# Performance work log

Measured on AMD Instinct MI355X. Metric: run time of the kernel, lower is better.

Reference implementation:

```python
import jax, jax.numpy as jnp
import numpy as np

N = 20000   # genes
E = 200000  # global edges
P = 300     # pathways
EP = 2000   # edges per pathway (global node indices)
D = 3       # in_dim == number of omics (forced by nn.Linear(3,1))


def setup_inputs():
    key = jax.random.key(0)
    ks = jax.random.split(key, 20)
    f = lambda i, shape: jax.random.normal(ks[i], shape, dtype=jnp.float32) * 0.1
    return {
        "x": f(0, (N, D)),
        "edge_index": jax.random.randint(ks[1], (2, E), 0, N),
        "path_edges": jax.random.randint(ks[2], (P, 2, EP), 0, N),
        "W_pool": f(3, (D, D)), "b_pool": f(4, (D,)),
        "W_self": f(5, (D, D)), "W_neigh": f(6, (D, D)), "b_conv": f(7, (D,)),
        "sub_Wl": f(8, (P, D, D)), "sub_bl": f(9, (P, D)), "sub_Wr": f(10, (P, D, D)),
        "pool_Wrel": f(11, (P, D, 1)), "pool_Wroot": f(12, (P, D, 1)), "pool_b": f(13, (P, 1)),
        "gate_W": f(14, (P, D, 1)), "gate_b": f(15, (P, 1)),
        "lin_W": f(16, (D, 1)), "lin_b": f(17, (1,)),
        "mlp_W": f(18, (P, 1)), "mlp_b": f(19, (1,)),
    }


def reference(x, edge_index, path_edges, W_pool, b_pool, W_self, W_neigh, b_conv,
              sub_Wl, sub_bl, sub_Wr, pool_Wrel, pool_Wroot, pool_b,
              gate_W, gate_b, lin_W, lin_b, mlp_W, mlp_b):
    n = x.shape[0]
    # add_self_loops on the global edge_index
    loops = jnp.arange(n)
    src = jnp.concatenate([edge_index[0], loops])
    dst = jnp.concatenate([edge_index[1], loops])

    # global SAGEConv with 'pool' aggregator: max_j relu(W_pool h_j), then self + neigh
    hp = jax.nn.relu(x @ W_pool + b_pool)                       # [N,D]
    agg = jax.ops.segment_max(hp[src], dst, num_segments=n)     # [N,D] (self-loops -> no empty segments)
    h = jnp.tanh(x @ W_self + agg @ W_neigh + b_conv)           # [N,D]

    k = int(np.ceil(0.8 * n))  # SAGPooling ratio=0.8 over all N nodes (full x is passed per pathway)

    def per_path(pe, Wl, bl, Wr, Wrel, Wroot, pb, gW, gb):
        s, d = pe[0], pe[1]
        # SAGEConv (mean aggr) on pathway subgraph edges over full node set
        msum = jax.ops.segment_sum(h[s], d, num_segments=n)
        cnt = jax.ops.segment_sum(jnp.ones(s.shape, h.dtype), d, num_segments=n)
        mean = msum / jnp.maximum(cnt, 1.0)[:, None]
        xc = jax.nn.relu(mean @ Wl + bl + h @ Wr)               # [N,D]
        # SAGPooling score via GraphConv (add aggr): W_rel * sum_j x_j + W_root * x + b
        asum = jax.ops.segment_sum(xc[s], d, num_segments=n)
        score = (asum @ Wrel + xc @ Wroot + pb)[:, 0]           # [N]
        topv, perm = jax.lax.top_k(score, k)
        xk = xc[perm] * jnp.tanh(topv)[:, None]                 # [k,D]
        # GlobalAttention readout: softmax gate over kept nodes
        gate = jax.nn.softmax((xk @ gW + gb)[:, 0])             # [k]
        return jax.nn.relu(gate @ xk)                            # [D]

    readout = jax.vmap(per_path)(path_edges, sub_Wl, sub_bl, sub_Wr,
                                 pool_Wrel, pool_Wroot, pool_b, gate_W, gate_b)  # [P,D]
    r = jax.nn.relu(readout @ lin_W + lin_b).T                  # [1,P]
    # mlp: Dropout (identity in eval) -> ReLU -> Linear(P,1) -> Sigmoid
    return jax.nn.sigmoid(jax.nn.relu(r) @ mlp_W + mlp_b)       # [1,1]
```

## Files before the change

### kernel.cpp

```cpp
#include <hip/hip_runtime.h>
#include <math.h>

#define MAXM 2048
#define BMW  640
#define BS   1024
#define NPT  20
#define NB   2048

__device__ __forceinline__ unsigned fkey(float f){
  unsigned u = __float_as_uint(f);
  return (u & 0x80000000u) ? ~u : (u | 0x80000000u);
}
__device__ __forceinline__ int lbin(float sc, float lo, float scl){
  int b = (int)((sc - lo) * scl);
  return b < 0 ? 0 : (b > NB-1 ? NB-1 : b);
}
__device__ __forceinline__ void hp_eval(const float* __restrict__ x, int i,
                                        const float* __restrict__ Wp,
                                        const float* __restrict__ bp, float* o){
  float x0 = x[i*3+0], x1 = x[i*3+1], x2 = x[i*3+2];
  #pragma unroll
  for (int j = 0; j < 3; ++j)
    o[j] = fmaxf(x0*Wp[0*3+j] + x1*Wp[1*3+j] + x2*Wp[2*3+j] + bp[j], 0.f);
}

__global__ void k_edge(const float* __restrict__ x, const int* __restrict__ ei,
                       const float* __restrict__ Wp, const float* __restrict__ bp,
                       float* __restrict__ agg, float* __restrict__ acc,
                       unsigned* __restrict__ counter, int E){
  if (blockIdx.x == 0 && threadIdx.x == 0){ acc[0] = 0.f; counter[0] = 0u; }
  int e = blockIdx.x*blockDim.x + threadIdx.x;
  if (e >= E) return;
  int s = ei[e], d = ei[E+e];
  float o[3]; hp_eval(x, s, Wp, bp, o);
  #pragma unroll
  for (int j = 0; j < 3; ++j)
    atomicMax((int*)&agg[d*3+j], __float_as_int(o[j]));
}

__global__ void k_h2(const float* __restrict__ x, const float* __restrict__ agg,
                     float4* __restrict__ h4,
                     const float* __restrict__ Wp, const float* __restrict__ bp,
                     const float* __restrict__ Ws, const float* __restrict__ Wn,
                     const float* __restrict__ bc, int N){
  int i = blockIdx.x*blockDim.x + threadIdx.x;
  if (i >= N) return;
  float hp[3]; hp_eval(x, i, Wp, bp, hp);
  float x0 = x[i*3+0], x1 = x[i*3+1], x2 = x[i*3+2];
  float a0 = fmaxf(agg[i*3+0], hp[0]);
  float a1 = fmaxf(agg[i*3+1], hp[1]);
  float a2 = fmaxf(agg[i*3+2], hp[2]);
  float o[3];
  #pragma unroll
  for (int j = 0; j < 3; ++j){
    float v = x0*Ws[0*3+j] + x1*Ws[1*3+j] + x2*Ws[2*3+j]
            + a0*Wn[0*3+j] + a1*Wn[1*3+j] + a2*Wn[2*3+j] + bc[j];
    o[j] = tanhf(v);
  }
  h4[i] = make_float4(o[0], o[1], o[2], 0.f);
}

__device__ __forceinline__ void pick_bucket(const unsigned* hist, int l,
    unsigned pref, unsigned mask, int shift,
    unsigned* sel_prefix, unsigned* sel_mask, int* sel_r){
  unsigned h0 = hist[4*l+0], h1 = hist[4*l+1], h2 = hist[4*l+2], h3 = hist[4*l+3];
  unsigned s = h0+h1+h2+h3;
  unsigned S = s;
  #pragma unroll
  for (int off = 1; off < 64; off <<= 1){
    unsigned t = __shfl_down(S, off);
    if (l + off < 64) S += t;
  }
  unsigned Snext = S - s;
  unsigned r = (unsigned)*sel_r;
  unsigned suf3 = h3 + Snext;
  unsigned suf2 = h2 + suf3;
  unsigned suf1 = h1 + suf2;
  unsigned suf0 = h0 + suf1;
  int b = -1; unsigned sufnext = 0;
  if      (suf3 >= r && Snext < r){ b = 4*l+3; sufnext = Snext; }
  else if (suf2 >= r && suf3  < r){ b = 4*l+2; sufnext = suf3; }
  else if (suf1 >= r && suf2  < r){ b = 4*l+1; sufnext = suf2; }
  else if (suf0 >= r && suf1  < r){ b = 4*l+0; sufnext = suf1; }
  if (b >= 0){
    *sel_prefix = pref | ((unsigned)b << shift);
    *sel_mask   = mask | (255u << shift);
    *sel_r      = (int)(r - sufnext);
  }
}

__global__ void __launch_bounds__(BS, 4)
k_mega(const float4* __restrict__ h4, const int* __restrict__ pe,
       const float* __restrict__ sWl, const float* __restrict__ sbl, const float* __restrict__ sWr,
       const float* __restrict__ pWrel, const float* __restrict__ pWroot, const float* __restrict__ pB,
       const float* __restrict__ gW, const float* __restrict__ gB,
       const float* __restrict__ linW, const float* __restrict__ linb,
       const float* __restrict__ mlpW, const float* __restrict__ mlpb,
       float* __restrict__ spG, float* __restrict__ acc, unsigned* __restrict__ counter,
       unsigned* __restrict__ out, int N, int EP, int K, int P){
  __shared__ unsigned bm[BMW];
  __shared__ int      wpfx[BMW];
  __shared__ float    msum[MAXM*3];
  __shared__ unsigned scrA[NB];
  __shared__ unsigned scrB[NB];
  __shared__ float    wredf[(BS/64)*4];
  __shared__ float    s_mn, s_mx;
  __shared__ float    rlo[3], rsc[3];
  __shared__ int      rb[3];
  __shared__ int      s_r, s_C, s_cc, s_done;
  __shared__ unsigned s_uT;
  __shared__ unsigned sel_prefix, sel_mask;
  __shared__ int      sel_r;

  const int p = blockIdx.x;
  const int tid = threadIdx.x;

  float Wl[9], Wr[9], bl[3], wrel[3], wroot[3], gw[3];
  #pragma unroll
  for (int j = 0; j < 9; ++j){ Wl[j] = sWl[p*9+j]; Wr[j] = sWr[p*9+j]; }
  #pragma unroll
  for (int j = 0; j < 3; ++j){
    bl[j] = sbl[p*3+j]; wrel[j] = pWrel[p*3+j];
    wroot[j] = pWroot[p*3+j]; gw[j] = gW[p*3+j];
  }
  float pbv = pB[p], gbv = gB[p];
  float* sp = spG + (size_t)p*N;

  int*   cnt  = (int*)scrA;
  float* adot = (float*)scrB;

  for (int s = tid; s < MAXM; s += BS){
    cnt[s] = 0; adot[s] = 0.f;
    msum[s*3+0]=0.f; msum[s*3+1]=0.f; msum[s*3+2]=0.f;
  }
  for (int s = tid; s < BMW; s += BS) bm[s] = 0u;
  if (tid == 0){ s_done = 0; s_uT = 0u; }
  __syncthreads();

  const int* ps = pe + (size_t)p*2*EP;
  const int* pd = ps + EP;

  for (int e = tid; e < EP; e += BS) atomicOr(&bm[pd[e]>>5], 1u << (pd[e]&31));
  __syncthreads();
  if (tid < 64){
    int l = tid, base = l*10;
    int c[10], s = 0;
    #pragma unroll
    for (int q = 0; q < 10; ++q){ c[q] = __popc(bm[base+q]); s += c[q]; }
    int pre = s;
    #pragma unroll
    for (int off = 1; off < 64; off <<= 1){
      int t = __shfl_up(pre, off);
      if (l >= off) pre += t;
    }
    pre -= s;
    #pragma unroll
    for (int q = 0; q < 10; ++q){ wpfx[base+q] = pre; pre += c[q]; }
  }
  __syncthreads();
  for (int e = tid; e < EP; e += BS){
    int s = ps[e], d = pd[e];
    int r = wpfx[d>>5] + __popc(bm[d>>5] & ((1u << (d&31)) - 1u));
    float4 hv = h4[s];
    atomicAdd(&cnt[r], 1);
    atomicAdd(&msum[r*3+0], hv.x);
    atomicAdd(&msum[r*3+1], hv.y);
    atomicAdd(&msum[r*3+2], hv.z);
  }
  __syncthreads();
  for (int r = tid; r < MAXM; r += BS){
    int c = cnt[r];
    if (c > 0){
      float inv = 1.f / (float)c;
      msum[r*3+0] *= inv; msum[r*3+1] *= inv; msum[r*3+2] *= inv;
    }
  }
  __syncthreads();
  for (int e = tid; e < EP; e += BS){
    int s = ps[e], d = pd[e];
    float m0=0.f,m1=0.f,m2=0.f;
    unsigned w = bm[s>>5];
    if ((w >> (s&31)) & 1u){
      int rs = wpfx[s>>5] + __popc(w & ((1u << (s&31)) - 1u));
      m0 = msum[rs*3+0]; m1 = msum[rs*3+1]; m2 = msum[rs*3+2];
    }
    float4 hv = h4[s];
    float x0 = fmaxf(m0*Wl[0]+m1*Wl[3]+m2*Wl[6] + bl[0] + hv.x*Wr[0]+hv.y*Wr[3]+hv.z*Wr[6], 0.f);
    float x1 = fmaxf(m0*Wl[1]+m1*Wl[4]+m2*Wl[7] + bl[1] + hv.x*Wr[1]+hv.y*Wr[4]+hv.z*Wr[7], 0.f);
    float x2 = fmaxf(m0*Wl[2]+m1*Wl[5]+m2*Wl[8] + bl[2] + hv.x*Wr[2]+hv.y*Wr[5]+hv.z*Wr[8], 0.f);
    int rd = wpfx[d>>5] + __popc(bm[d>>5] & ((1u << (d&31)) - 1u));
    atomicAdd(&adot[rd], x0*wrel[0] + x1*wrel[1] + x2*wrel[2]);
  }
  __syncthreads();

  float scq[NPT];
  float mn = 3.0e38f, mx = -3.0e38f;
  #pragma unroll
  for (int j = 0; j < NPT; ++j){
    int i = tid + j*BS;
    float sc = 0.f;
    if (i < N){
      float m0=0.f,m1=0.f,m2=0.f,ad=0.f;
      unsigned w = bm[i>>5];
      if ((w >> (i&31)) & 1u){
        int r = wpfx[i>>5] + __popc(w & ((1u << (i&31)) - 1u));
        m0 = msum[r*3+0]; m1 = msum[r*3+1]; m2 = msum[r*3+2];
        ad = adot[r];
      }
      float4 hv = h4[i];
      float x0 = fmaxf(m0*Wl[0]+m1*Wl[3]+m2*Wl[6] + bl[0] + hv.x*Wr[0]+hv.y*Wr[3]+hv.z*Wr[6], 0.f);
      float x1 = fmaxf(m0*Wl[1]+m1*Wl[4]+m2*Wl[7] + bl[1] + hv.x*Wr[1]+hv.y*Wr[4]+hv.z*Wr[7], 0.f);
      float x2 = fmaxf(m0*Wl[2]+m1*Wl[5]+m2*Wl[8] + bl[2] + hv.x*Wr[2]+hv.y*Wr[5]+hv.z*Wr[8], 0.f);
      sc = ad + x0*wroot[0]+x1*wroot[1]+x2*wroot[2] + pbv;
      mn = fminf(mn, sc); mx = fmaxf(mx, sc);
    }
    scq[j] = sc;
  }
  for (int i = BS*NPT + tid; i < N; i += BS){
    float m0=0.f,m1=0.f,m2=0.f,ad=0.f;
    unsigned w = bm[i>>5];
    if ((w >> (i&31)) & 1u){
      int r = wpfx[i>>5] + __popc(w & ((1u << (i&31)) - 1u));
      m0 = msum[r*3+0]; m1 = msum[r*3+1]; m2 = msum[r*3+2];
      ad = adot[r];
    }
    float4 hv = h4[i];
    float x0 = fmaxf(m0*Wl[0]+m1*Wl[3]+m2*Wl[6] + bl[0] + hv.x*Wr[0]+hv.y*Wr[3]+hv.z*Wr[6], 0.f);
    float x1 = fmaxf(m0*Wl[1]+m1*Wl[4]+m2*Wl[7] + bl[1] + hv.x*Wr[1]+hv.y*Wr[4]+hv.z*Wr[7], 0.f);
    float x2 = fmaxf(m0*Wl[2]+m1*Wl[5]+m2*Wl[8] + bl[2] + hv.x*Wr[2]+hv.y*Wr[5]+hv.z*Wr[8], 0.f);
    float sc = ad + x0*wroot[0]+x1*wroot[1]+x2*wroot[2] + pbv;
    sp[i] = sc;
    mn = fminf(mn, sc); mx = fmaxf(mx, sc);
  }
  #pragma unroll
  for (int off = 32; off > 0; off >>= 1){
    mn = fminf(mn, __shfl_down(mn, off));
    mx = fmaxf(mx, __shfl_down(mx, off));
  }
  if ((tid & 63) == 0){ int w = tid>>6; wredf[w*2+0] = mn; wredf[w*2+1] = mx; }
  __syncthreads();
  if (tid == 0){
    float a = 3.0e38f, b = -3.0e38f;
    for (int w = 0; w < BS/64; ++w){ a = fminf(a, wredf[w*2+0]); b = fmaxf(b, wredf[w*2+1]); }
    s_mn = a; s_mx = b; s_r = K;
    if (!(b > a)){ s_uT = fkey(a); s_done = 1; }
  }
  __syncthreads();

  unsigned* hist = scrA;
  unsigned* cand = scrB;

  for (int t = 0; t < 3; ++t){
    __syncthreads();
    if (s_done) break;
    float lo, hi;
    if (t == 0){ lo = s_mn; hi = s_mx; }
    else { lo = rlo[t-1] + rb[t-1]/rsc[t-1]; hi = rlo[t-1] + (rb[t-1]+1)/rsc[t-1]; }
    float scl = 2047.0f / (hi - lo);
    if (!(hi > lo) || !(scl < 1e37f)){
      if (tid == 0){ s_uT = fkey(lo); s_done = 1; }
      __syncthreads();
      continue;
    }
    for (int b = tid; b < NB; b += BS) hist[b] = 0u;
    __syncthreads();
    #pragma unroll
    for (int j = 0; j < NPT; ++j){
      int i = tid + j*BS;
      if (i < N){
        float sc = scq[j];
        bool act = true;
        for (int q = 0; q < t; ++q) act = act && (lbin(sc, rlo[q], rsc[q]) == rb[q]);
        if (act) atomicAdd(&hist[lbin(sc, lo, scl)], 1u);
      }
    }
    for (int i = BS*NPT + tid; i < N; i += BS){
      float sc = sp[i];
      bool act = true;
      for (int q = 0; q < t; ++q) act = act && (lbin(sc, rlo[q], rsc[q]) == rb[q]);
      if (act) atomicAdd(&hist[lbin(sc, lo, scl)], 1u);
    }
    __syncthreads();
    if (tid < 64){
      int l = tid;
      unsigned s = 0;
      for (int q = 0; q < 32; ++q) s += hist[l*32+q];
      unsigned S = s;
      #pragma unroll
      for (int off = 1; off < 64; off <<= 1){
        unsigned u2 = __shfl_down(S, off);
        if (l + off < 64) S += u2;
      }
      unsigned suf = S - s;
      unsigned r = (unsigned)s_r;
      int b = -1; unsigned sufnext = 0, cb = 0;
      for (int q = 31; q >= 0; --q){
        unsigned c = hist[l*32+q];
        unsigned nsuf = suf + c;
        if (nsuf >= r && suf < r){ b = l*32+q; sufnext = suf; cb = c; }
        suf = nsuf;
      }
      if (b >= 0){
        rb[t] = b; rlo[t] = lo; rsc[t] = scl;
        s_r = (int)(r - sufnext);
        s_C = (int)cb;
      }
    }
    __syncthreads();
    int C = s_C;
    if (C <= NB){
      if (tid == 0) s_cc = 0;
      __syncthreads();
      #pragma unroll
      for (int j = 0; j < NPT; ++j){
        int i = tid + j*BS;
        if (i < N){
          float sc = scq[j];
          bool act = true;
          for (int q = 0; q <= t; ++q) act = act && (lbin(sc, rlo[q], rsc[q]) == rb[q]);
          if (act){ int ix = atomicAdd(&s_cc, 1); if (ix < NB) cand[ix] = fkey(sc); }
        }
      }
      for (int i = BS*NPT + tid; i < N; i += BS){
        float sc = sp[i];
        bool act = true;
        for (int q = 0; q <= t; ++q) act = act && (lbin(sc, rlo[q], rsc[q]) == rb[q]);
        if (act){ int ix = atomicAdd(&s_cc, 1); if (ix < NB) cand[ix] = fkey(sc); }
      }
      __syncthreads();
      if (tid == 0){ sel_prefix = 0u; sel_mask = 0u; sel_r = s_r; }
      __syncthreads();
      for (int pass = 0; pass < 4; ++pass){
        int shift = 24 - 8*pass;
        if (tid < 256) hist[tid] = 0u;
        __syncthreads();
        unsigned mask = sel_mask, pref = sel_prefix;
        for (int j = tid; j < C; j += BS){
          unsigned u = cand[j];
          if ((u & mask) == pref) atomicAdd(&hist[(u>>shift)&255u], 1u);
        }
        __syncthreads();
        if (tid < 64)
          pick_bucket(hist, tid, pref, mask, shift, &sel_prefix, &sel_mask, &sel_r);
        __syncthreads();
      }
      if (tid == 0){ s_uT = sel_prefix; s_done = 1; }
      __syncthreads();
    } else if (t == 2){
      if (tid == 0){ s_uT = fkey(lo + rb[t]/scl); s_done = 1; }
      __syncthreads();
    }
  }
  __syncthreads();
  const unsigned uT = s_uT;

  float l = 0.f, a0 = 0.f, a1 = 0.f, a2 = 0.f;
  #pragma unroll
  for (int j = 0; j < NPT; ++j){
    int i = tid + j*BS;
    if (i < N && fkey(scq[j]) >= uT){
      float sc = scq[j];
      float m0=0.f,m1=0.f,m2=0.f;
      unsigned w = bm[i>>5];
      if ((w >> (i&31)) & 1u){
        int r = wpfx[i>>5] + __popc(w & ((1u << (i&31)) - 1u));
        m0 = msum[r*3+0]; m1 = msum[r*3+1]; m2 = msum[r*3+2];
      }
      float4 hv = h4[i];
      float x0 = fmaxf(m0*Wl[0]+m1*Wl[3]+m2*Wl[6] + bl[0] + hv.x*Wr[0]+hv.y*Wr[3]+hv.z*Wr[6], 0.f);
      float x1 = fmaxf(m0*Wl[1]+m1*Wl[4]+m2*Wl[7] + bl[1] + hv.x*Wr[1]+hv.y*Wr[4]+hv.z*Wr[7], 0.f);
      float x2 = fmaxf(m0*Wl[2]+m1*Wl[5]+m2*Wl[8] + bl[2] + hv.x*Wr[2]+hv.y*Wr[5]+hv.z*Wr[8], 0.f);
      float tt = tanhf(sc);
      x0 *= tt; x1 *= tt; x2 *= tt;
      float g = x0*gw[0] + x1*gw[1] + x2*gw[2] + gbv;
      g = fminf(fmaxf(g, -60.f), 60.f);
      float e = expf(g);
      l += e; a0 += e*x0; a1 += e*x1; a2 += e*x2;
    }
  }
  for (int i = BS*NPT + tid; i < N; i += BS){
    float sc = sp[i];
    if (fkey(sc) >= uT){
      float m0=0.f,m1=0.f,m2=0.f;
      unsigned w = bm[i>>5];
      if ((w >> (i&31)) & 1u){
        int r = wpfx[i>>5] + __popc(w & ((1u << (i&31)) - 1u));
        m0 = msum[r*3+0]; m1 = msum[r*3+1]; m2 = msum[r*3+2];
      }
      float4 hv = h4[i];
      float x0 = fmaxf(m0*Wl[0]+m1*Wl[3]+m2*Wl[6] + bl[0] + hv.x*Wr[0]+hv.y*Wr[3]+hv.z*Wr[6], 0.f);
      float x1 = fmaxf(m0*Wl[1]+m1*Wl[4]+m2*Wl[7] + bl[1] + hv.x*Wr[1]+hv.y*Wr[4]+hv.z*Wr[7], 0.f);
      float x2 = fmaxf(m0*Wl[2]+m1*Wl[5]+m2*Wl[8] + bl[2] + hv.x*Wr[2]+hv.y*Wr[5]+hv.z*Wr[8], 0.f);
      float tt = tanhf(sc);
      x0 *= tt; x1 *= tt; x2 *= tt;
      float g = x0*gw[0] + x1*gw[1] + x2*gw[2] + gbv;
      g = fminf(fmaxf(g, -60.f), 60.f);
      float e = expf(g);
      l += e; a0 += e*x0; a1 += e*x1; a2 += e*x2;
    }
  }
  #pragma unroll
  for (int off = 32; off > 0; off >>= 1){
    l  += __shfl_down(l,  off);
    a0 += __shfl_down(a0, off);
    a1 += __shfl_down(a1, off);
    a2 += __shfl_down(a2, off);
  }
  if ((tid & 63) == 0){
    int w = tid >> 6;
    wredf[w*4+0]=l; wredf[w*4+1]=a0; wredf[w*4+2]=a1; wredf[w*4+3]=a2;
  }
  __syncthreads();
  if (tid == 0){
    float L=0.f, A0=0.f, A1=0.f, A2=0.f;
    for (int w = 0; w < BS/64; ++w){
      L += wredf[w*4+0]; A0 += wredf[w*4+1]; A1 += wredf[w*4+2]; A2 += wredf[w*4+3];
    }
    float inv = 1.f / L;
    float r0 = fmaxf(A0*inv, 0.f);
    float r1 = fmaxf(A1*inv, 0.f);
    float r2 = fmaxf(A2*inv, 0.f);
    float rr = fmaxf(r0*linW[0] + r1*linW[1] + r2*linW[2] + linb[0], 0.f);
    atomicAdd(acc, rr * mlpW[p]);
    __threadfence();
    unsigned old = atomicAdd(counter, 1u);
    if (old == (unsigned)(P-1)){
      __threadfence();
      float z = atomicAdd(acc, 0.f) + mlpb[0];
      float a = 1.f / (1.f + expf(-z));
      unsigned A = __float_as_uint(a);
      unsigned B = (A + 0x7FFFu + ((A >> 16) & 1u)) >> 16;
      out[0] = (A & 0xFFFF0000u) | (B & 0xFFFFu);
    }
  }
}

extern "C" void kernel_launch(void* const* d_in, const int* in_sizes, int n_in,
                              void* d_out, int out_size, void* d_ws, size_t ws_size,
                              hipStream_t stream){
  const float* x      = (const float*)d_in[0];
  const int*   ei     = (const int*)  d_in[1];
  const int*   pe     = (const int*)  d_in[2];
  const float* W_pool = (const float*)d_in[3];
  const float* b_pool = (const float*)d_in[4];
  const float* W_self = (const float*)d_in[5];
  const float* W_neigh= (const float*)d_in[6];
  const float* b_conv = (const float*)d_in[7];
  const float* sWl    = (const float*)d_in[8];
  const float* sbl    = (const float*)d_in[9];
  const float* sWr    = (const float*)d_in[10];
  const float* pWrel  = (const float*)d_in[11];
  const float* pWroot = (const float*)d_in[12];
  const float* pB     = (const float*)d_in[13];
  const float* gW     = (const float*)d_in[14];
  const float* gB     = (const float*)d_in[15];
  const float* linW   = (const float*)d_in[16];
  const float* linb   = (const float*)d_in[17];
  const float* mlpW   = (const float*)d_in[18];
  const float* mlpb   = (const float*)d_in[19];

  const int N  = in_sizes[0] / 3;
  const int E  = in_sizes[1] / 2;
  const int P  = in_sizes[13];
  const int EP = in_sizes[2] / (2 * P);
  const int K  = (4*N + 4) / 5;

  float*    ws      = (float*)d_ws;
  float*    acc     = ws;
  unsigned* counter = (unsigned*)(ws + 1);
  float*    agg     = ws + 16;
  size_t    o_h4    = (16 + (size_t)3*N + 3) & ~(size_t)3;
  float4*   h4      = (float4*)(ws + o_h4);
  float*    spG     = ws + o_h4 + (size_t)4*N;

  k_edge<<<(E+255)/256, 256, 0, stream>>>(x, ei, W_pool, b_pool, agg, acc, counter, E);
  k_h2  <<<(N+255)/256, 256, 0, stream>>>(x, agg, h4, W_pool, b_pool,
                                          W_self, W_neigh, b_conv, N);
  k_mega<<<P, BS, 0, stream>>>(h4, pe, sWl, sbl, sWr, pWrel, pWroot, pB, gW, gB,
                               linW, linb, mlpW, mlpb,
                               spG, acc, counter, (unsigned*)d_out, N, EP, K, P);
}
```

Before: 256.1 us.

## Shrink per-block LDS in pathway kernel to fit more blocks per CU

Cuts the pathway kernel's shared memory by moving per-node edge counts to a global buffer (zeroed by a memset), storing mean features as bf16 in a reused region, shortening the prefix table to 16-bit, and halving the histogram bins. Block size drops to 512 threads with 40 scores per thread in registers. The goal is lower LDS per block so more of the 300 pathway blocks stay resident per CU. The cost is global atomics for counts, bf16 rounding error on the mean features, coarser top-k binning that may need more refinement passes, and higher register pressure from the larger per-thread score array.

```diff
diff --git a/kernel.cpp b/kernel.cpp
--- a/kernel.cpp
+++ b/kernel.cpp
@@ -1,11 +1,11 @@
 #include <hip/hip_runtime.h>
 #include <math.h>
 
-#define MAXM 2048
+#define MAXM 2000
 #define BMW  640
-#define BS   1024
-#define NPT  20
-#define NB   2048
+#define BS   512
+#define NPT  40
+#define NB   1024
 
 __device__ __forceinline__ unsigned fkey(float f){
   unsigned u = __float_as_uint(f);
@@ -14,6 +14,13 @@
 __device__ __forceinline__ int lbin(float sc, float lo, float scl){
   int b = (int)((sc - lo) * scl);
   return b < 0 ? 0 : (b > NB-1 ? NB-1 : b);
+}
+__device__ __forceinline__ unsigned short benc(float f){
+  unsigned A = __float_as_uint(f);
+  return (unsigned short)((A + 0x7FFFu + ((A >> 16) & 1u)) >> 16);
+}
+__device__ __forceinline__ float bdec(unsigned short u){
+  return __uint_as_float(((unsigned)u) << 16);
 }
 __device__ __forceinline__ void hp_eval(const float* __restrict__ x, int i,
                                         const float* __restrict__ Wp,
@@ -96,21 +103,17 @@
        const float* __restrict__ gW, const float* __restrict__ gB,
        const float* __restrict__ linW, const float* __restrict__ linb,
        const float* __restrict__ mlpW, const float* __restrict__ mlpb,
-       float* __restrict__ spG, float* __restrict__ acc, unsigned* __restrict__ counter,
+       int* __restrict__ cntG, float* __restrict__ spG,
+       float* __restrict__ acc, unsigned* __restrict__ counter,
        unsigned* __restrict__ out, int N, int EP, int K, int P){
-  __shared__ unsigned bm[BMW];
-  __shared__ int      wpfx[BMW];
-  __shared__ float    msum[MAXM*3];
-  __shared__ unsigned scrA[NB];
-  __shared__ unsigned scrB[NB];
-  __shared__ float    wredf[(BS/64)*4];
-  __shared__ float    s_mn, s_mx;
-  __shared__ float    rlo[3], rsc[3];
-  __shared__ int      rb[3];
-  __shared__ int      s_r, s_C, s_cc, s_done;
-  __shared__ unsigned s_uT;
-  __shared__ unsigned sel_prefix, sel_mask;
-  __shared__ int      sel_r;
+  __shared__ unsigned       bm[BMW];
+  __shared__ unsigned short wpfx[BMW];
+  __shared__ float          Xf[6000];
+  __shared__ float          wredf[64];
+  __shared__ float s_mn, s_mx, rlo[3], rsc[3];
+  __shared__ int   rb[3], s_r, s_C, s_cc, s_done;
+  __shared__ unsigned s_uT, sel_prefix, sel_mask;
+  __shared__ int   sel_r;
 
   const int p = blockIdx.x;
   const int tid = threadIdx.x;
@@ -125,14 +128,15 @@
   }
   float pbv = pB[p], gbv = gB[p];
   float* sp = spG + (size_t)p*N;
-
-  int*   cnt  = (int*)scrA;
-  float* adot = (float*)scrB;
-
-  for (int s = tid; s < MAXM; s += BS){
-    cnt[s] = 0; adot[s] = 0.f;
-    msum[s*3+0]=0.f; msum[s*3+1]=0.f; msum[s*3+2]=0.f;
-  }
+  int*   cntP = cntG + (size_t)p*MAXM;
+
+  float*          msum  = Xf;
+  unsigned short* msumh = (unsigned short*)Xf;
+  float*          adot  = Xf + 3000;
+  unsigned*       hist  = (unsigned*)(Xf + 3000);
+  unsigned*       cand  = (unsigned*)(Xf + 3000) + NB;
+
+  for (int s = tid; s < 6000; s += BS) msum[s] = 0.f;
   for (int s = tid; s < BMW; s += BS) bm[s] = 0u;
   if (tid == 0){ s_done = 0; s_uT = 0u; }
   __syncthreads();
@@ -155,25 +159,37 @@
     }
     pre -= s;
     #pragma unroll
-    for (int q = 0; q < 10; ++q){ wpfx[base+q] = pre; pre += c[q]; }
+    for (int q = 0; q < 10; ++q){ wpfx[base+q] = (unsigned short)pre; pre += c[q]; }
   }
   __syncthreads();
   for (int e = tid; e < EP; e += BS){
     int s = ps[e], d = pd[e];
-    int r = wpfx[d>>5] + __popc(bm[d>>5] & ((1u << (d&31)) - 1u));
+    int r = (int)wpfx[d>>5] + __popc(bm[d>>5] & ((1u << (d&31)) - 1u));
     float4 hv = h4[s];
-    atomicAdd(&cnt[r], 1);
+    atomicAdd(&cntP[r], 1);
     atomicAdd(&msum[r*3+0], hv.x);
     atomicAdd(&msum[r*3+1], hv.y);
     atomicAdd(&msum[r*3+2], hv.z);
   }
   __syncthreads();
-  for (int r = tid; r < MAXM; r += BS){
-    int c = cnt[r];
-    if (c > 0){
-      float inv = 1.f / (float)c;
-      msum[r*3+0] *= inv; msum[r*3+1] *= inv; msum[r*3+2] *= inv;
-    }
+  {
+    float tmpv[12];
+    int nr = 0;
+    for (int r = tid; r < MAXM; r += BS, ++nr){
+      int c = atomicAdd(&cntP[r], 0);
+      float inv = (c > 0) ? 1.f/(float)c : 0.f;
+      tmpv[nr*3+0] = msum[r*3+0]*inv;
+      tmpv[nr*3+1] = msum[r*3+1]*inv;
+      tmpv[nr*3+2] = msum[r*3+2]*inv;
+    }
+    __syncthreads();
+    nr = 0;
+    for (int r = tid; r < MAXM; r += BS, ++nr){
+      msumh[r*3+0] = benc(tmpv[nr*3+0]);
+      msumh[r*3+1] = benc(tmpv[nr*3+1]);
+      msumh[r*3+2] = benc(tmpv[nr*3+2]);
+    }
+    for (int s = tid; s < MAXM; s += BS) adot[s] = 0.f;
   }
   __syncthreads();
   for (int e = tid; e < EP; e += BS){
@@ -181,14 +197,14 @@
     float m0=0.f,m1=0.f,m2=0.f;
     unsigned w = bm[s>>5];
     if ((w >> (s&31)) & 1u){
-      int rs = wpfx[s>>5] + __popc(w & ((1u << (s&31)) - 1u));
-      m0 = msum[rs*3+0]; m1 = msum[rs*3+1]; m2 = msum[rs*3+2];
+      int rs = (int)wpfx[s>>5] + __popc(w & ((1u << (s&31)) - 1u));
+      m0 = bdec(msumh[rs*3+0]); m1 = bdec(msumh[rs*3+1]); m2 = bdec(msumh[rs*3+2]);
     }
     float4 hv = h4[s];
     float x0 = fmaxf(m0*Wl[0]+m1*Wl[3]+m2*Wl[6] + bl[0] + hv.x*Wr[0]+hv.y*Wr[3]+hv.z*Wr[6], 0.f);
     float x1 = fmaxf(m0*Wl[1]+m1*Wl[4]+m2*Wl[7] + bl[1] + hv.x*Wr[1]+hv.y*Wr[4]+hv.z*Wr[7], 0.f);
     float x2 = fmaxf(m0*Wl[2]+m1*Wl[5]+m2*Wl[8] + bl[2] + hv.x*Wr[2]+hv.y*Wr[5]+hv.z*Wr[8], 0.f);
-    int rd = wpfx[d>>5] + __popc(bm[d>>5] & ((1u << (d&31)) - 1u));
+    int rd = (int)wpfx[d>>5] + __popc(bm[d>>5] & ((1u << (d&31)) - 1u));
     atomicAdd(&adot[rd], x0*wrel[0] + x1*wrel[1] + x2*wrel[2]);
   }
   __syncthreads();
@@ -203,8 +219,8 @@
       float m0=0.f,m1=0.f,m2=0.f,ad=0.f;
       unsigned w = bm[i>>5];
       if ((w >> (i&31)) & 1u){
-        int r = wpfx[i>>5] + __popc(w & ((1u << (i&31)) - 1u));
-        m0 = msum[r*3+0]; m1 = msum[r*3+1]; m2 = msum[r*3+2];
+        int r = (int)wpfx[i>>5] + __popc(w & ((1u << (i&31)) - 1u));
+        m0 = bdec(msumh[r*3+0]); m1 = bdec(msumh[r*3+1]); m2 = bdec(msumh[r*3+2]);
         ad = adot[r];
       }
       float4 hv = h4[i];
@@ -220,8 +236,8 @@
     float m0=0.f,m1=0.f,m2=0.f,ad=0.f;
     unsigned w = bm[i>>5];
     if ((w >> (i&31)) & 1u){
-      int r = wpfx[i>>5] + __popc(w & ((1u << (i&31)) - 1u));
-      m0 = msum[r*3+0]; m1 = msum[r*3+1]; m2 = msum[r*3+2];
+      int r = (int)wpfx[i>>5] + __popc(w & ((1u << (i&31)) - 1u));
+      m0 = bdec(msumh[r*3+0]); m1 = bdec(msumh[r*3+1]); m2 = bdec(msumh[r*3+2]);
       ad = adot[r];
     }
     float4 hv = h4[i];
@@ -247,16 +263,13 @@
   }
   __syncthreads();
 
-  unsigned* hist = scrA;
-  unsigned* cand = scrB;
-
   for (int t = 0; t < 3; ++t){
     __syncthreads();
     if (s_done) break;
     float lo, hi;
     if (t == 0){ lo = s_mn; hi = s_mx; }
     else { lo = rlo[t-1] + rb[t-1]/rsc[t-1]; hi = rlo[t-1] + (rb[t-1]+1)/rsc[t-1]; }
-    float scl = 2047.0f / (hi - lo);
+    float scl = (float)(NB-1) / (hi - lo);
     if (!(hi > lo) || !(scl < 1e37f)){
       if (tid == 0){ s_uT = fkey(lo); s_done = 1; }
       __syncthreads();
@@ -284,7 +297,7 @@
     if (tid < 64){
       int l = tid;
       unsigned s = 0;
-      for (int q = 0; q < 32; ++q) s += hist[l*32+q];
+      for (int q = 0; q < 16; ++q) s += hist[l*16+q];
       unsigned S = s;
       #pragma unroll
       for (int off = 1; off < 64; off <<= 1){
@@ -294,10 +307,10 @@
       unsigned suf = S - s;
       unsigned r = (unsigned)s_r;
       int b = -1; unsigned sufnext = 0, cb = 0;
-      for (int q = 31; q >= 0; --q){
-        unsigned c = hist[l*32+q];
+      for (int q = 15; q >= 0; --q){
+        unsigned c = hist[l*16+q];
         unsigned nsuf = suf + c;
-        if (nsuf >= r && suf < r){ b = l*32+q; sufnext = suf; cb = c; }
+        if (nsuf >= r && suf < r){ b = l*16+q; sufnext = suf; cb = c; }
         suf = nsuf;
       }
       if (b >= 0){
@@ -363,8 +376,8 @@
       float m0=0.f,m1=0.f,m2=0.f;
       unsigned w = bm[i>>5];
       if ((w >> (i&31)) & 1u){
-        int r = wpfx[i>>5] + __popc(w & ((1u << (i&31)) - 1u));
-        m0 = msum[r*3+0]; m1 = msum[r*3+1]; m2 = msum[r*3+2];
+        int r = (int)wpfx[i>>5] + __popc(w & ((1u << (i&31)) - 1u));
+        m0 = bdec(msumh[r*3+0]); m1 = bdec(msumh[r*3+1]); m2 = bdec(msumh[r*3+2]);
       }
       float4 hv = h4[i];
       float x0 = fmaxf(m0*Wl[0]+m1*Wl[3]+m2*Wl[6] + bl[0] + hv.x*Wr[0]+hv.y*Wr[3]+hv.z*Wr[6], 0.f);
@@ -384,8 +397,8 @@
       float m0=0.f,m1=0.f,m2=0.f;
       unsigned w = bm[i>>5];
       if ((w >> (i&31)) & 1u){
-        int r = wpfx[i>>5] + __popc(w & ((1u << (i&31)) - 1u));
-        m0 = msum[r*3+0]; m1 = msum[r*3+1]; m2 = msum[r*3+2];
+        int r = (int)wpfx[i>>5] + __popc(w & ((1u << (i&31)) - 1u));
+        m0 = bdec(msumh[r*3+0]); m1 = bdec(msumh[r*3+1]); m2 = bdec(msumh[r*3+2]);
       }
       float4 hv = h4[i];
       float x0 = fmaxf(m0*Wl[0]+m1*Wl[3]+m2*Wl[6] + bl[0] + hv.x*Wr[0]+hv.y*Wr[3]+hv.z*Wr[6], 0.f);
@@ -472,11 +485,13 @@
   size_t    o_h4    = (16 + (size_t)3*N + 3) & ~(size_t)3;
   float4*   h4      = (float4*)(ws + o_h4);
   float*    spG     = ws + o_h4 + (size_t)4*N;
-
+  int*      cntG    = (int*)(spG + (size_t)P*N);
+
+  hipMemsetAsync(cntG, 0, (size_t)P*MAXM*sizeof(int), stream);
   k_edge<<<(E+255)/256, 256, 0, stream>>>(x, ei, W_pool, b_pool, agg, acc, counter, E);
   k_h2  <<<(N+255)/256, 256, 0, stream>>>(x, agg, h4, W_pool, b_pool,
                                           W_self, W_neigh, b_conv, N);
   k_mega<<<P, BS, 0, stream>>>(h4, pe, sWl, sbl, sWr, pWrel, pWroot, pB, gW, gB,
                                linW, linb, mlpW, mlpb,
-                               spG, acc, counter, (unsigned*)d_out, N, EP, K, P);
-}
+                               cntG, spG, acc, counter, (unsigned*)d_out, N, EP, K, P);
+}
```

Result: no change. 257.0 us (+0.3%).
